# Kernel optimization log

Hardware: AMD Instinct MI355X
Metric: run time of the kernel (lower is better)

Reference implementation:

```python
import jax, jax.numpy as jnp
import numpy as np
import math

M, INPUT_DIM, CLASSES, LATENT = 4096, 64, 10, 2

# ---- Bessel-approximation phi functions (Abramowitz & Stegun polynomial series) ----

def phi_f(s):
    t = s / 7.5
    t2 = t * t
    poly = 1.0 + 3.5156229 * t2 + 3.0899424 * t2**2 + 1.2067492 * t2**3 \
         + 0.2659732 * t2**4 + 0.0360768 * t2**5 + 0.0045813 * t2**6
    return jnp.exp(-s / 2.0) * poly


def phi_g(s):
    t = s / 7.5
    u = 1.0 / t  # s >= 7.5 when called via phi, so t >= 1
    poly = 0.39894228 + 0.01328592 * u + 0.00225319 * u**2 - 0.00157565 * u**3 \
         + 0.0091628 * u**4 - 0.02057706 * u**5 + 0.02635537 * u**6 \
         - 0.01647633 * u**7 + 0.00392377 * u**8
    return jnp.sqrt(2.0 / s) * poly


def phi(x):
    a = jnp.float32(7.5)
    return phi_f(jnp.minimum(x, a)) - phi_f(a) + phi_g(jnp.maximum(x, a))


def phi_d(s, D):
    if D <= 2:
        return phi(s)
    return 1.0 / jnp.sqrt(1.0 + 4.0 * s / (2 * D - 3))


def cramer_wold_distance(X, mu, variance, p, gamma):
    m, K = X.shape
    variance_matrix = variance[None, :] + variance[:, None]          # [C, C]
    # A term: pairwise latent-sample distances [m, m]
    A1 = jnp.sum((X[None, :, :] - X[:, None, :]) ** 2, axis=-1)      # [m, m]
    A = jnp.sum(phi_d(A1 / (4.0 * gamma), K)) / (m * m * math.sqrt(2.0 * math.pi * 2.0 * gamma))
    # B term: sample-to-mean distances [m, C]
    B1 = jnp.sum((mu[None, :, :] - X[:, None, :]) ** 2, axis=-1)     # [m, C]
    B2 = phi_d(B1 / (2.0 * (variance + 2.0 * gamma)), K)
    B = jnp.sum(2.0 * p / (m * jnp.sqrt(2.0 * math.pi * (variance + 2.0 * gamma))) * B2)
    # C term: mean-to-mean distances [C, C]
    C1 = jnp.sum((mu[None, :, :] - mu[:, None, :]) ** 2, axis=-1)
    C2 = phi_d(C1 / (2.0 * variance_matrix + 4.0 * gamma), K)
    C3 = jnp.outer(p, p) / jnp.sqrt(2.0 * math.pi * (variance_matrix + 2.0 * gamma))
    C = jnp.sum(C3 * C2)
    return A - B + C


def setup_inputs() -> dict:
    key = jax.random.key(0)
    ks = jax.random.split(key, 12)
    tau = jax.random.normal(ks[0], (M, INPUT_DIM), dtype=jnp.float32)
    # first half of batch is labeled (one-hot), second half unlabeled (zeros)
    lab_idx = jax.random.randint(ks[1], (M // 2,), 0, CLASSES)
    labels = jnp.concatenate([jax.nn.one_hot(lab_idx, CLASSES, dtype=jnp.float32),
                              jnp.zeros((M - M // 2, CLASSES), jnp.float32)], axis=0)
    batch_data = jnp.concatenate([tau, labels], axis=1)

    def xavier(k, fan_in, fan_out):
        lim = math.sqrt(6.0 / (fan_in + fan_out))
        return jax.random.uniform(k, (fan_in, fan_out), jnp.float32, -lim, lim)

    inp = {
        'batch_data': batch_data,
        'We1': xavier(ks[2], INPUT_DIM, 32), 'be1': jnp.zeros((32,), jnp.float32),
        'We2': xavier(ks[3], 32, 16),        'be2': jnp.zeros((16,), jnp.float32),
        'We3': xavier(ks[4], 16, LATENT),    'be3': jnp.zeros((LATENT,), jnp.float32),
        'Wd1': xavier(ks[5], LATENT, 16),    'bd1': jnp.zeros((16,), jnp.float32),
        'Wd2': xavier(ks[6], 16, 32),        'bd2': jnp.zeros((32,), jnp.float32),
        'Wd3': xavier(ks[7], 32, INPUT_DIM), 'bd3': jnp.zeros((INPUT_DIM,), jnp.float32),
        # GMM: init=2.0, gauss_num <= z_dim branch not taken (10 > 2) -> N(0, init)
        'means': 2.0 * jax.random.normal(ks[8], (CLASSES, LATENT), jnp.float32),
        'variances': jnp.ones((CLASSES,), jnp.float32),
        'probs': jnp.full((CLASSES,), 1.0 / CLASSES, jnp.float32),
    }
    return inp


def segma_forward(batch_data, We1, be1, We2, be2, We3, be3,
                  Wd1, bd1, Wd2, bd2, Wd3, bd3, means, variances, probs):
    tau = batch_data[:, :INPUT_DIM]
    labels = batch_data[:, INPUT_DIM:]
    # encoder
    x = jnp.tanh(tau @ We1 + be1)
    x = jnp.tanh(x @ We2 + be2)
    z = x @ We3 + be3                                               # [m, K]
    # decoder
    h = jnp.tanh(z @ Wd1 + bd1)
    h = jnp.tanh(h @ Wd2 + bd2)
    tau_decoded = h @ Wd3 + bd3
    rec_loss = jnp.mean((tau - tau_decoded) ** 2)
    # labeled mask: rows whose one-hot labels sum to exactly 1
    labeled_mask = (jnp.sum(labels, axis=-1) == 1.0)
    # class logits: Gaussian log-likelihood under each mixture component
    D = means.shape[-1]
    sq = jnp.sum((z[:, None, :] - means[None, :, :]) ** 2, axis=-1)  # [m, C]
    class_logits = jnp.log(probs) - 0.5 * D * jnp.log(2.0 * math.pi * variances) - sq / (2.0 * variances)
    # cross-entropy with (soft/one-hot) float targets, masked to labeled rows
    ce = -jnp.sum(labels * jax.nn.log_softmax(class_logits, axis=-1), axis=-1)
    den = jnp.sum(labels)
    den = jnp.where(den == 0, 1.0, den)
    class_loss = jnp.sum(ce * labeled_mask.astype(jnp.float32)) / den
    # Cramer-Wold cost (train_labeled=True -> use all z)
    m = z.shape[0]
    gamma = jnp.float32((4.0 / (3.0 * m)) ** 0.2)
    cw_cost = cramer_wold_distance(z, means, variances, probs, gamma)
    log_cw_cost = 8.0 + jnp.log(cw_cost)
    total_loss = rec_loss + 1.0 * log_cw_cost + 2.0 * class_loss
    return total_loss


def reference(batch_data, We1, be1, We2, be2, We3, be3,
              Wd1, bd1, Wd2, bd2, Wd3, bd3, means, variances, probs):
    return segma_forward(batch_data, We1, be1, We2, be2, We3, be3,
                         Wd1, bd1, Wd2, bd2, Wd3, bd3, means, variances, probs)
```

## Files before the change

kernel.cpp:

```cpp
#include <hip/hip_runtime.h>
#include <math.h>

#define M_ROWS 4096
#define IN_DIM 64
#define NCLS 10
#define ROW_STRIDE 74
#define TWO_PI_F 6.283185307179586f
#define NTILE 64
#define NPAIR 2080

__device__ __forceinline__ float phi_f_eval(float s) {
    float t = s * (1.0f / 7.5f);
    float t2 = t * t;
    float p = 0.0045813f;
    p = fmaf(p, t2, 0.0360768f);
    p = fmaf(p, t2, 0.2659732f);
    p = fmaf(p, t2, 1.2067492f);
    p = fmaf(p, t2, 3.0899424f);
    p = fmaf(p, t2, 3.5156229f);
    p = fmaf(p, t2, 1.0f);
    return __expf(-0.5f * s) * p;
}

__device__ __forceinline__ float phi_g_eval(float s) {
    float r = __builtin_amdgcn_rcpf(s);
    float u = 7.5f * r;
    float p = 0.00392377f;
    p = fmaf(p, u, -0.01647633f);
    p = fmaf(p, u, 0.02635537f);
    p = fmaf(p, u, -0.02057706f);
    p = fmaf(p, u, 0.0091628f);
    p = fmaf(p, u, -0.00157565f);
    p = fmaf(p, u, 0.00225319f);
    p = fmaf(p, u, 0.01328592f);
    p = fmaf(p, u, 0.39894228f);
    return __builtin_amdgcn_sqrtf(2.0f * r) * p;
}

#define PHI_F_75 0.21445709f

__device__ __forceinline__ float phi_eval(float s) {
    float f = phi_f_eval(fminf(s, 7.5f));
    float g = phi_g_eval(fmaxf(s, 7.5f));
    return f - PHI_F_75 + g;
}

__device__ __forceinline__ float fast_tanh(float x) {
    float e = __expf(2.0f * x);
    float r = __builtin_amdgcn_rcpf(e + 1.0f);
    return fmaf(-2.0f, r, 1.0f);
}

__device__ __forceinline__ float waveReduce(float v) {
    v += __shfl_down(v, 32, 64);
    v += __shfl_down(v, 16, 64);
    v += __shfl_down(v, 8, 64);
    v += __shfl_down(v, 4, 64);
    v += __shfl_down(v, 2, 64);
    v += __shfl_down(v, 1, 64);
    return v;
}

__device__ __forceinline__ double waveReduceD(double v) {
    v += __shfl_down(v, 32, 64);
    v += __shfl_down(v, 16, 64);
    v += __shfl_down(v, 8, 64);
    v += __shfl_down(v, 4, 64);
    v += __shfl_down(v, 2, 64);
    v += __shfl_down(v, 1, 64);
    return v;
}

#define O_W1T   0
#define O_W2T   2048
#define O_WD2T  2560
#define O_WD3T  3072
#define O_W3T   5120
#define O_WD1T  5152
#define O_B1    5184
#define O_B2    5216
#define O_B3    5232
#define O_BD1   5236
#define O_BD2   5252
#define O_BD3   5284
#define O_MU    5348
#define O_VAR   5368
#define O_PRB   5378
#define SM_TOT  5392

__global__ __launch_bounds__(64, 1) void k_mlp(
    const float* __restrict__ batch,
    const float* __restrict__ We1, const float* __restrict__ be1,
    const float* __restrict__ We2, const float* __restrict__ be2,
    const float* __restrict__ We3, const float* __restrict__ be3,
    const float* __restrict__ Wd1, const float* __restrict__ bd1,
    const float* __restrict__ Wd2, const float* __restrict__ bd2,
    const float* __restrict__ Wd3, const float* __restrict__ bd3,
    const float* __restrict__ means, const float* __restrict__ vars,
    const float* __restrict__ probs,
    float2* __restrict__ zbuf,
    float* __restrict__ recp, float* __restrict__ Bp,
    float* __restrict__ clsp, float* __restrict__ labp,
    float gamma)
{
    __shared__ __align__(16) float sm[SM_TOT];
    const int tid = threadIdx.x;

    for (int idx = tid; idx < 2048; idx += 64) { int i = idx >> 5, j = idx & 31; sm[O_W1T + j * 64 + i] = We1[idx]; }
    for (int idx = tid; idx < 512;  idx += 64) { int i = idx >> 4, j = idx & 15; sm[O_W2T + j * 32 + i] = We2[idx]; }
    for (int idx = tid; idx < 512;  idx += 64) { int i = idx >> 5, j = idx & 31; sm[O_WD2T + j * 16 + i] = Wd2[idx]; }
    for (int idx = tid; idx < 2048; idx += 64) { int i = idx >> 6, j = idx & 63; sm[O_WD3T + j * 32 + i] = Wd3[idx]; }
    if (tid < 32) { int i = tid >> 1, j = tid & 1;  sm[O_W3T + j * 16 + i] = We3[tid]; }
    else          { int t2 = tid - 32; int i = t2 >> 4, j = t2 & 15; sm[O_WD1T + j * 2 + i] = Wd1[t2]; }
    if (tid < 32) sm[O_B1 + tid] = be1[tid];
    if (tid < 16) sm[O_B2 + tid] = be2[tid];
    if (tid < 2)  sm[O_B3 + tid] = be3[tid];
    if (tid < 16) sm[O_BD1 + tid] = bd1[tid];
    if (tid < 32) sm[O_BD2 + tid] = bd2[tid];
    sm[O_BD3 + tid] = bd3[tid];
    if (tid < 20) sm[O_MU + tid] = means[tid];
    if (tid < 10) sm[O_VAR + tid] = vars[tid];
    if (tid < 10) sm[O_PRB + tid] = probs[tid];
    __syncthreads();

    const int row = blockIdx.x * 64 + tid;
    const float* rp = batch + (size_t)row * ROW_STRIDE;

    float tau[64];
#pragma unroll
    for (int i = 0; i < 32; i++) {
        float2 v = ((const float2*)rp)[i];
        tau[2 * i] = v.x; tau[2 * i + 1] = v.y;
    }

    float x1[32];
#pragma unroll
    for (int j = 0; j < 32; j++) {
        const float4* w = (const float4*)&sm[O_W1T + j * 64];
        float acc = sm[O_B1 + j];
#pragma unroll
        for (int i = 0; i < 16; i++) {
            float4 wv = w[i];
            acc = fmaf(tau[4 * i],     wv.x, acc);
            acc = fmaf(tau[4 * i + 1], wv.y, acc);
            acc = fmaf(tau[4 * i + 2], wv.z, acc);
            acc = fmaf(tau[4 * i + 3], wv.w, acc);
        }
        x1[j] = fast_tanh(acc);
    }

    float x2[16];
#pragma unroll
    for (int j = 0; j < 16; j++) {
        const float4* w = (const float4*)&sm[O_W2T + j * 32];
        float acc = sm[O_B2 + j];
#pragma unroll
        for (int i = 0; i < 8; i++) {
            float4 wv = w[i];
            acc = fmaf(x1[4 * i],     wv.x, acc);
            acc = fmaf(x1[4 * i + 1], wv.y, acc);
            acc = fmaf(x1[4 * i + 2], wv.z, acc);
            acc = fmaf(x1[4 * i + 3], wv.w, acc);
        }
        x2[j] = fast_tanh(acc);
    }

    float z0 = sm[O_B3 + 0], z1 = sm[O_B3 + 1];
#pragma unroll
    for (int i = 0; i < 16; i++) {
        z0 = fmaf(x2[i], sm[O_W3T + 0 * 16 + i], z0);
        z1 = fmaf(x2[i], sm[O_W3T + 1 * 16 + i], z1);
    }
    zbuf[row] = make_float2(z0, z1);

    float h1[16];
#pragma unroll
    for (int j = 0; j < 16; j++) {
        float acc = sm[O_BD1 + j];
        acc = fmaf(z0, sm[O_WD1T + j * 2 + 0], acc);
        acc = fmaf(z1, sm[O_WD1T + j * 2 + 1], acc);
        h1[j] = fast_tanh(acc);
    }

    float h2[32];
#pragma unroll
    for (int j = 0; j < 32; j++) {
        const float4* w = (const float4*)&sm[O_WD2T + j * 16];
        float acc = sm[O_BD2 + j];
#pragma unroll
        for (int i = 0; i < 4; i++) {
            float4 wv = w[i];
            acc = fmaf(h1[4 * i],     wv.x, acc);
            acc = fmaf(h1[4 * i + 1], wv.y, acc);
            acc = fmaf(h1[4 * i + 2], wv.z, acc);
            acc = fmaf(h1[4 * i + 3], wv.w, acc);
        }
        h2[j] = fast_tanh(acc);
    }

    float rec = 0.0f;
#pragma unroll
    for (int o = 0; o < 64; o++) {
        const float4* w = (const float4*)&sm[O_WD3T + o * 32];
        float acc = sm[O_BD3 + o];
#pragma unroll
        for (int i = 0; i < 8; i++) {
            float4 wv = w[i];
            acc = fmaf(h2[4 * i],     wv.x, acc);
            acc = fmaf(h2[4 * i + 1], wv.y, acc);
            acc = fmaf(h2[4 * i + 2], wv.z, acc);
            acc = fmaf(h2[4 * i + 3], wv.w, acc);
        }
        float e = acc - tau[o];
        rec = fmaf(e, e, rec);
    }

    const float two_g = 2.0f * gamma;
    const float inv_m = 1.0f / (float)M_ROWS;
    float lg[NCLS];
    float mx = -3.0e38f;
    float Bacc = 0.0f;
#pragma unroll
    for (int c = 0; c < NCLS; c++) {
        float d0 = z0 - sm[O_MU + 2 * c];
        float d1 = z1 - sm[O_MU + 2 * c + 1];
        float sqc = fmaf(d0, d0, d1 * d1);
        float vc = sm[O_VAR + c];
        float lgc = __logf(sm[O_PRB + c]) - __logf(TWO_PI_F * vc)
                    - sqc * 0.5f * __builtin_amdgcn_rcpf(vc);
        lg[c] = lgc;
        mx = fmaxf(mx, lgc);

        float den = vc + two_g;
        float sB = sqc * 0.5f * __builtin_amdgcn_rcpf(den);
        float coef = 2.0f * inv_m * sm[O_PRB + c] * __builtin_amdgcn_rsqf(TWO_PI_F * den);
        Bacc = fmaf(coef, phi_eval(sB), Bacc);
    }
    float esum = 0.0f;
#pragma unroll
    for (int c = 0; c < NCLS; c++) esum += __expf(lg[c] - mx);
    float lse = __logf(esum) + mx;

    float suml = 0.0f, ce = 0.0f;
#pragma unroll
    for (int c = 0; c < NCLS; c++) {
        float lb = rp[IN_DIM + c];
        suml += lb;
        ce = fmaf(lb, lse - lg[c], ce);
    }
    float cls = (suml == 1.0f) ? ce : 0.0f;

    float r0 = waveReduce(rec);
    float r1 = waveReduce(Bacc);
    float r2 = waveReduce(cls);
    float r3 = waveReduce(suml);
    if (tid == 0) {
        recp[blockIdx.x] = r0;
        Bp[blockIdx.x]   = r1;
        clsp[blockIdx.x] = r2;
        labp[blockIdx.x] = r3;
    }
}

__global__ __launch_bounds__(64, 4) void k_pair(
    const float2* __restrict__ z, float* __restrict__ Apart, float inv4g)
{
    const int p = blockIdx.x;
    int tj = (int)((__builtin_amdgcn_sqrtf(8.0f * (float)p + 1.0f) - 1.0f) * 0.5f);
    while ((tj + 1) * (tj + 2) / 2 <= p) tj++;
    while (tj * (tj + 1) / 2 > p) tj--;
    const int ti = p - tj * (tj + 1) / 2;

    const int lane = threadIdx.x;
    __shared__ float2 zjs[64];
    float2 zi = z[ti * 64 + lane];
    zjs[lane] = z[tj * 64 + lane];
    __syncthreads();

    float acc0 = 0.0f, acc1 = 0.0f;
#pragma unroll 8
    for (int jj = 0; jj < 64; jj += 2) {
        float2 a = zjs[jj], b = zjs[jj + 1];
        float dx0 = zi.x - a.x, dy0 = zi.y - a.y;
        float dx1 = zi.x - b.x, dy1 = zi.y - b.y;
        acc0 += phi_eval(fmaf(dx0, dx0, dy0 * dy0) * inv4g);
        acc1 += phi_eval(fmaf(dx1, dx1, dy1 * dy1) * inv4g);
    }
    float tot = waveReduce(acc0 + acc1);
    if (lane == 0) Apart[p] = (ti == tj) ? tot : 2.0f * tot;
}

__global__ __launch_bounds__(256) void k_fin(
    const float* __restrict__ means, const float* __restrict__ vars,
    const float* __restrict__ probs,
    const float* __restrict__ Apart,
    const float* __restrict__ recp, const float* __restrict__ Bp,
    const float* __restrict__ clsp, const float* __restrict__ labp,
    float* __restrict__ out, float gamma)
{
    __shared__ double wsum[8];
    const int t = threadIdx.x;
    const int w = t >> 6;

    const double m = (double)M_ROWS;
    const double gam = (double)gamma;
    const double invA = 1.0 / (m * m * sqrt(2.0 * M_PI * 2.0 * gam));

    double av = 0.0;
#pragma unroll
    for (int k = 0; k < 9; k++) {
        int idx = t + 256 * k;
        if (idx < NPAIR) av += (double)Apart[idx];
    }

    double cv = 0.0;
    if (t < 100) {
        int ci = t / 10, cj = t - 10 * (t / 10);
        float vm = vars[ci] + vars[cj];
        float d0 = means[2 * ci] - means[2 * cj];
        float d1 = means[2 * ci + 1] - means[2 * cj + 1];
        float c1 = fmaf(d0, d0, d1 * d1);
        float s = c1 / (2.0f * vm + 4.0f * gamma);
        float c2 = phi_eval(s);
        float c3 = probs[ci] * probs[cj] * __builtin_amdgcn_rsqf(TWO_PI_F * (vm + 2.0f * gamma));
        cv = (double)(c3 * c2);
    }

    double acw = waveReduceD(av * invA + cv);

    const int l = t & 63;
    double pv;
    if (w == 0)      pv = (double)recp[l];
    else if (w == 1) pv = (double)Bp[l];
    else if (w == 2) pv = (double)clsp[l];
    else             pv = (double)labp[l];
    double pw = waveReduceD(pv);

    if (l == 0) { wsum[w] = acw; wsum[4 + w] = pw; }
    __syncthreads();

    if (t == 0) {
        double AC = wsum[0] + wsum[1] + wsum[2] + wsum[3];
        double rec = wsum[4], B = wsum[5], cls = wsum[6], lab = wsum[7];
        double den = (lab == 0.0) ? 1.0 : lab;
        double cw = AC - B;
        double total = rec / (m * 64.0) + 8.0 + log(cw) + 2.0 * (cls / den);
        out[0] = (float)total;
    }
}

extern "C" void kernel_launch(void* const* d_in, const int* in_sizes, int n_in,
                              void* d_out, int out_size, void* d_ws, size_t ws_size,
                              hipStream_t stream) {
    (void)in_sizes; (void)n_in; (void)out_size; (void)ws_size;
    const float* batch = (const float*)d_in[0];
    const float* We1 = (const float*)d_in[1];
    const float* be1 = (const float*)d_in[2];
    const float* We2 = (const float*)d_in[3];
    const float* be2 = (const float*)d_in[4];
    const float* We3 = (const float*)d_in[5];
    const float* be3 = (const float*)d_in[6];
    const float* Wd1 = (const float*)d_in[7];
    const float* bd1 = (const float*)d_in[8];
    const float* Wd2 = (const float*)d_in[9];
    const float* bd2 = (const float*)d_in[10];
    const float* Wd3 = (const float*)d_in[11];
    const float* bd3 = (const float*)d_in[12];
    const float* means = (const float*)d_in[13];
    const float* vars = (const float*)d_in[14];
    const float* probs = (const float*)d_in[15];

    float* ws = (float*)d_ws;
    float2* zbuf = (float2*)ws;
    float* Apart = ws + 8192;
    float* recp  = ws + 12288;
    float* Bp    = ws + 12352;
    float* clsp  = ws + 12416;
    float* labp  = ws + 12480;

    const float gamma = (float)pow(4.0 / (3.0 * (double)M_ROWS), 0.2);
    const float inv4g = 1.0f / (4.0f * gamma);

    k_mlp<<<64, 64, 0, stream>>>(batch, We1, be1, We2, be2, We3, be3,
                                 Wd1, bd1, Wd2, bd2, Wd3, bd3,
                                 means, vars, probs,
                                 zbuf, recp, Bp, clsp, labp, gamma);
    k_pair<<<NPAIR, 64, 0, stream>>>(zbuf, Apart, inv4g);
    k_fin<<<1, 256, 0, stream>>>(means, vars, probs, Apart, recp, Bp, clsp, labp,
                                 (float*)d_out, gamma);
}
```

Measured before the change: 131.4 us.

## Split each MLP row across four lanes with shuffle reductions, use 256 blocks

The encoder/decoder MLP now assigns four lanes per row: each lane handles a quarter of the input features, accumulates partial outputs for all neurons, then combines them with xor shuffles and keeps its own slice of neurons. Weights are stored row-major with padding in shared memory to suit this access pattern. The grid grows from 64 to 256 blocks, so more of the GPU is occupied, and the finisher reads 256 partials per quantity instead of 64. The cost is many extra shuffles per layer, redundant per-row class and B computation across lanes, and more per-lane accumulator registers.

```diff
diff --git a/kernel.cpp b/kernel.cpp
--- a/kernel.cpp
+++ b/kernel.cpp
@@ -8,6 +8,7 @@
 #define TWO_PI_F 6.283185307179586f
 #define NTILE 64
 #define NPAIR 2080
+#define NBLK_MLP 256
 
 __device__ __forceinline__ float phi_f_eval(float s) {
     float t = s * (1.0f / 7.5f);
@@ -71,22 +72,28 @@
     return v;
 }
 
-#define O_W1T   0
-#define O_W2T   2048
-#define O_WD2T  2560
-#define O_WD3T  3072
-#define O_W3T   5120
-#define O_WD1T  5152
-#define O_B1    5184
-#define O_B2    5216
-#define O_B3    5232
-#define O_BD1   5236
-#define O_BD2   5252
-#define O_BD3   5284
-#define O_MU    5348
-#define O_VAR   5368
-#define O_PRB   5378
-#define SM_TOT  5392
+__device__ __forceinline__ float sel4(float v0, float v1, float v2, float v3, int r) {
+    float a = (r & 1) ? v1 : v0;
+    float b = (r & 1) ? v3 : v2;
+    return (r & 2) ? b : a;
+}
+
+#define P_W1   0
+#define P_W2   2304
+#define P_WD2  2944
+#define P_WD3  3520
+#define P_W3   5696
+#define P_WD1  5728
+#define P_B1   5760
+#define P_B2   5792
+#define P_B3   5808
+#define P_BD1  5810
+#define P_BD2  5826
+#define P_BD3  5858
+#define P_MU   5922
+#define P_VAR  5942
+#define P_PRB  5952
+#define SMT    5962
 
 __global__ __launch_bounds__(64, 1) void k_mlp(
     const float* __restrict__ batch,
@@ -103,115 +110,170 @@
     float* __restrict__ clsp, float* __restrict__ labp,
     float gamma)
 {
-    __shared__ __align__(16) float sm[SM_TOT];
+    __shared__ __align__(16) float sm[SMT];
     const int tid = threadIdx.x;
 
-    for (int idx = tid; idx < 2048; idx += 64) { int i = idx >> 5, j = idx & 31; sm[O_W1T + j * 64 + i] = We1[idx]; }
-    for (int idx = tid; idx < 512;  idx += 64) { int i = idx >> 4, j = idx & 15; sm[O_W2T + j * 32 + i] = We2[idx]; }
-    for (int idx = tid; idx < 512;  idx += 64) { int i = idx >> 5, j = idx & 31; sm[O_WD2T + j * 16 + i] = Wd2[idx]; }
-    for (int idx = tid; idx < 2048; idx += 64) { int i = idx >> 6, j = idx & 63; sm[O_WD3T + j * 32 + i] = Wd3[idx]; }
-    if (tid < 32) { int i = tid >> 1, j = tid & 1;  sm[O_W3T + j * 16 + i] = We3[tid]; }
-    else          { int t2 = tid - 32; int i = t2 >> 4, j = t2 & 15; sm[O_WD1T + j * 2 + i] = Wd1[t2]; }
-    if (tid < 32) sm[O_B1 + tid] = be1[tid];
-    if (tid < 16) sm[O_B2 + tid] = be2[tid];
-    if (tid < 2)  sm[O_B3 + tid] = be3[tid];
-    if (tid < 16) sm[O_BD1 + tid] = bd1[tid];
-    if (tid < 32) sm[O_BD2 + tid] = bd2[tid];
-    sm[O_BD3 + tid] = bd3[tid];
-    if (tid < 20) sm[O_MU + tid] = means[tid];
-    if (tid < 10) sm[O_VAR + tid] = vars[tid];
-    if (tid < 10) sm[O_PRB + tid] = probs[tid];
+    for (int idx = tid; idx < 2048; idx += 64) { int i = idx >> 5, j = idx & 31; sm[P_W1  + i * 36 + j] = We1[idx]; }
+    for (int idx = tid; idx < 512;  idx += 64) { int i = idx >> 4, j = idx & 15; sm[P_W2  + i * 20 + j] = We2[idx]; }
+    for (int idx = tid; idx < 512;  idx += 64) { int i = idx >> 5, j = idx & 31; sm[P_WD2 + i * 36 + j] = Wd2[idx]; }
+    for (int idx = tid; idx < 2048; idx += 64) { int i = idx >> 6, j = idx & 63; sm[P_WD3 + i * 68 + j] = Wd3[idx]; }
+    if (tid < 32) sm[P_W3 + tid] = We3[tid];
+    else          sm[P_WD1 + tid - 32] = Wd1[tid - 32];
+    if (tid < 32) sm[P_B1 + tid] = be1[tid];
+    if (tid < 16) sm[P_B2 + tid] = be2[tid];
+    if (tid < 2)  sm[P_B3 + tid] = be3[tid];
+    if (tid < 16) sm[P_BD1 + tid] = bd1[tid];
+    if (tid < 32) sm[P_BD2 + tid] = bd2[tid];
+    sm[P_BD3 + tid] = bd3[tid];
+    if (tid < 20) sm[P_MU + tid] = means[tid];
+    if (tid < 10) sm[P_VAR + tid] = vars[tid];
+    if (tid < 10) sm[P_PRB + tid] = probs[tid];
     __syncthreads();
 
-    const int row = blockIdx.x * 64 + tid;
+    const int rw = tid & 15;
+    const int r  = tid >> 4;
+    const int row = blockIdx.x * 16 + rw;
     const float* rp = batch + (size_t)row * ROW_STRIDE;
 
-    float tau[64];
-#pragma unroll
-    for (int i = 0; i < 32; i++) {
-        float2 v = ((const float2*)rp)[i];
-        tau[2 * i] = v.x; tau[2 * i + 1] = v.y;
-    }
-
-    float x1[32];
+    float taus[16];
+#pragma unroll
+    for (int k = 0; k < 16; k++) taus[k] = rp[r + 4 * k];
+
+    float a1[32];
+#pragma unroll
+    for (int j = 0; j < 32; j++) a1[j] = 0.0f;
+#pragma unroll
+    for (int k = 0; k < 16; k++) {
+        const int i = r + 4 * k;
+        const float4* wr = (const float4*)&sm[P_W1 + i * 36];
+        const float ti = taus[k];
+#pragma unroll
+        for (int jj = 0; jj < 8; jj++) {
+            float4 w = wr[jj];
+            a1[4 * jj + 0] = fmaf(ti, w.x, a1[4 * jj + 0]);
+            a1[4 * jj + 1] = fmaf(ti, w.y, a1[4 * jj + 1]);
+            a1[4 * jj + 2] = fmaf(ti, w.z, a1[4 * jj + 2]);
+            a1[4 * jj + 3] = fmaf(ti, w.w, a1[4 * jj + 3]);
+        }
+    }
 #pragma unroll
     for (int j = 0; j < 32; j++) {
-        const float4* w = (const float4*)&sm[O_W1T + j * 64];
-        float acc = sm[O_B1 + j];
-#pragma unroll
-        for (int i = 0; i < 16; i++) {
-            float4 wv = w[i];
-            acc = fmaf(tau[4 * i],     wv.x, acc);
-            acc = fmaf(tau[4 * i + 1], wv.y, acc);
-            acc = fmaf(tau[4 * i + 2], wv.z, acc);
-            acc = fmaf(tau[4 * i + 3], wv.w, acc);
+        a1[j] += __shfl_xor(a1[j], 16, 64);
+        a1[j] += __shfl_xor(a1[j], 32, 64);
+    }
+    float x1own[8];
+#pragma unroll
+    for (int k = 0; k < 8; k++)
+        x1own[k] = fast_tanh(sel4(a1[4 * k], a1[4 * k + 1], a1[4 * k + 2], a1[4 * k + 3], r)
+                             + sm[P_B1 + r + 4 * k]);
+
+    float a2[16];
+#pragma unroll
+    for (int j = 0; j < 16; j++) a2[j] = 0.0f;
+#pragma unroll
+    for (int k = 0; k < 8; k++) {
+        const int i = r + 4 * k;
+        const float4* wr = (const float4*)&sm[P_W2 + i * 20];
+        const float x = x1own[k];
+#pragma unroll
+        for (int jj = 0; jj < 4; jj++) {
+            float4 w = wr[jj];
+            a2[4 * jj + 0] = fmaf(x, w.x, a2[4 * jj + 0]);
+            a2[4 * jj + 1] = fmaf(x, w.y, a2[4 * jj + 1]);
+            a2[4 * jj + 2] = fmaf(x, w.z, a2[4 * jj + 2]);
+            a2[4 * jj + 3] = fmaf(x, w.w, a2[4 * jj + 3]);
         }
-        x1[j] = fast_tanh(acc);
-    }
-
-    float x2[16];
+    }
 #pragma unroll
     for (int j = 0; j < 16; j++) {
-        const float4* w = (const float4*)&sm[O_W2T + j * 32];
-        float acc = sm[O_B2 + j];
-#pragma unroll
-        for (int i = 0; i < 8; i++) {
-            float4 wv = w[i];
-            acc = fmaf(x1[4 * i],     wv.x, acc);
-            acc = fmaf(x1[4 * i + 1], wv.y, acc);
-            acc = fmaf(x1[4 * i + 2], wv.z, acc);
-            acc = fmaf(x1[4 * i + 3], wv.w, acc);
+        a2[j] += __shfl_xor(a2[j], 16, 64);
+        a2[j] += __shfl_xor(a2[j], 32, 64);
+    }
+    float x2own[4];
+#pragma unroll
+    for (int k = 0; k < 4; k++)
+        x2own[k] = fast_tanh(sel4(a2[4 * k], a2[4 * k + 1], a2[4 * k + 2], a2[4 * k + 3], r)
+                             + sm[P_B2 + r + 4 * k]);
+
+    float z0 = 0.0f, z1 = 0.0f;
+#pragma unroll
+    for (int k = 0; k < 4; k++) {
+        const int i = r + 4 * k;
+        z0 = fmaf(x2own[k], sm[P_W3 + 2 * i], z0);
+        z1 = fmaf(x2own[k], sm[P_W3 + 2 * i + 1], z1);
+    }
+    z0 += __shfl_xor(z0, 16, 64); z0 += __shfl_xor(z0, 32, 64);
+    z1 += __shfl_xor(z1, 16, 64); z1 += __shfl_xor(z1, 32, 64);
+    z0 += sm[P_B3 + 0];
+    z1 += sm[P_B3 + 1];
+    if (r == 0) zbuf[row] = make_float2(z0, z1);
+
+    float h1own[4];
+#pragma unroll
+    for (int k = 0; k < 4; k++) {
+        const int j = r + 4 * k;
+        float acc = sm[P_BD1 + j];
+        acc = fmaf(z0, sm[P_WD1 + j], acc);
+        acc = fmaf(z1, sm[P_WD1 + 16 + j], acc);
+        h1own[k] = fast_tanh(acc);
+    }
+
+    float a3[32];
+#pragma unroll
+    for (int j = 0; j < 32; j++) a3[j] = 0.0f;
+#pragma unroll
+    for (int k = 0; k < 4; k++) {
+        const int i = r + 4 * k;
+        const float4* wr = (const float4*)&sm[P_WD2 + i * 36];
+        const float x = h1own[k];
+#pragma unroll
+        for (int jj = 0; jj < 8; jj++) {
+            float4 w = wr[jj];
+            a3[4 * jj + 0] = fmaf(x, w.x, a3[4 * jj + 0]);
+            a3[4 * jj + 1] = fmaf(x, w.y, a3[4 * jj + 1]);
+            a3[4 * jj + 2] = fmaf(x, w.z, a3[4 * jj + 2]);
+            a3[4 * jj + 3] = fmaf(x, w.w, a3[4 * jj + 3]);
         }
-        x2[j] = fast_tanh(acc);
-    }
-
-    float z0 = sm[O_B3 + 0], z1 = sm[O_B3 + 1];
-#pragma unroll
-    for (int i = 0; i < 16; i++) {
-        z0 = fmaf(x2[i], sm[O_W3T + 0 * 16 + i], z0);
-        z1 = fmaf(x2[i], sm[O_W3T + 1 * 16 + i], z1);
-    }
-    zbuf[row] = make_float2(z0, z1);
-
-    float h1[16];
-#pragma unroll
-    for (int j = 0; j < 16; j++) {
-        float acc = sm[O_BD1 + j];
-        acc = fmaf(z0, sm[O_WD1T + j * 2 + 0], acc);
-        acc = fmaf(z1, sm[O_WD1T + j * 2 + 1], acc);
-        h1[j] = fast_tanh(acc);
-    }
-
-    float h2[32];
+    }
 #pragma unroll
     for (int j = 0; j < 32; j++) {
-        const float4* w = (const float4*)&sm[O_WD2T + j * 16];
-        float acc = sm[O_BD2 + j];
-#pragma unroll
-        for (int i = 0; i < 4; i++) {
-            float4 wv = w[i];
-            acc = fmaf(h1[4 * i],     wv.x, acc);
-            acc = fmaf(h1[4 * i + 1], wv.y, acc);
-            acc = fmaf(h1[4 * i + 2], wv.z, acc);
-            acc = fmaf(h1[4 * i + 3], wv.w, acc);
+        a3[j] += __shfl_xor(a3[j], 16, 64);
+        a3[j] += __shfl_xor(a3[j], 32, 64);
+    }
+    float h2own[8];
+#pragma unroll
+    for (int k = 0; k < 8; k++)
+        h2own[k] = fast_tanh(sel4(a3[4 * k], a3[4 * k + 1], a3[4 * k + 2], a3[4 * k + 3], r)
+                             + sm[P_BD2 + r + 4 * k]);
+
+    float a4[64];
+#pragma unroll
+    for (int j = 0; j < 64; j++) a4[j] = 0.0f;
+#pragma unroll
+    for (int k = 0; k < 8; k++) {
+        const int i = r + 4 * k;
+        const float4* wr = (const float4*)&sm[P_WD3 + i * 68];
+        const float x = h2own[k];
+#pragma unroll
+        for (int jj = 0; jj < 16; jj++) {
+            float4 w = wr[jj];
+            a4[4 * jj + 0] = fmaf(x, w.x, a4[4 * jj + 0]);
+            a4[4 * jj + 1] = fmaf(x, w.y, a4[4 * jj + 1]);
+            a4[4 * jj + 2] = fmaf(x, w.z, a4[4 * jj + 2]);
+            a4[4 * jj + 3] = fmaf(x, w.w, a4[4 * jj + 3]);
         }
-        h2[j] = fast_tanh(acc);
-    }
-
+    }
+#pragma unroll
+    for (int j = 0; j < 64; j++) {
+        a4[j] += __shfl_xor(a4[j], 16, 64);
+        a4[j] += __shfl_xor(a4[j], 32, 64);
+    }
     float rec = 0.0f;
 #pragma unroll
-    for (int o = 0; o < 64; o++) {
-        const float4* w = (const float4*)&sm[O_WD3T + o * 32];
-        float acc = sm[O_BD3 + o];
-#pragma unroll
-        for (int i = 0; i < 8; i++) {
-            float4 wv = w[i];
-            acc = fmaf(h2[4 * i],     wv.x, acc);
-            acc = fmaf(h2[4 * i + 1], wv.y, acc);
-            acc = fmaf(h2[4 * i + 2], wv.z, acc);
-            acc = fmaf(h2[4 * i + 3], wv.w, acc);
-        }
-        float e = acc - tau[o];
+    for (int k = 0; k < 16; k++) {
+        float dec = sel4(a4[4 * k], a4[4 * k + 1], a4[4 * k + 2], a4[4 * k + 3], r)
+                    + sm[P_BD3 + r + 4 * k];
+        float e = dec - taus[k];
         rec = fmaf(e, e, rec);
     }
 
@@ -222,18 +284,18 @@
     float Bacc = 0.0f;
 #pragma unroll
     for (int c = 0; c < NCLS; c++) {
-        float d0 = z0 - sm[O_MU + 2 * c];
-        float d1 = z1 - sm[O_MU + 2 * c + 1];
+        float d0 = z0 - sm[P_MU + 2 * c];
+        float d1 = z1 - sm[P_MU + 2 * c + 1];
         float sqc = fmaf(d0, d0, d1 * d1);
-        float vc = sm[O_VAR + c];
-        float lgc = __logf(sm[O_PRB + c]) - __logf(TWO_PI_F * vc)
+        float vc = sm[P_VAR + c];
+        float lgc = __logf(sm[P_PRB + c]) - __logf(TWO_PI_F * vc)
                     - sqc * 0.5f * __builtin_amdgcn_rcpf(vc);
         lg[c] = lgc;
         mx = fmaxf(mx, lgc);
 
         float den = vc + two_g;
         float sB = sqc * 0.5f * __builtin_amdgcn_rcpf(den);
-        float coef = 2.0f * inv_m * sm[O_PRB + c] * __builtin_amdgcn_rsqf(TWO_PI_F * den);
+        float coef = 2.0f * inv_m * sm[P_PRB + c] * __builtin_amdgcn_rsqf(TWO_PI_F * den);
         Bacc = fmaf(coef, phi_eval(sB), Bacc);
     }
     float esum = 0.0f;
@@ -249,6 +311,7 @@
         ce = fmaf(lb, lse - lg[c], ce);
     }
     float cls = (suml == 1.0f) ? ce : 0.0f;
+    if (r != 0) { Bacc = 0.0f; cls = 0.0f; suml = 0.0f; }
 
     float r0 = waveReduce(rec);
     float r1 = waveReduce(Bacc);
@@ -301,6 +364,7 @@
     __shared__ double wsum[8];
     const int t = threadIdx.x;
     const int w = t >> 6;
+    const int l = t & 63;
 
     const double m = (double)M_ROWS;
     const double gam = (double)gamma;
@@ -328,12 +392,10 @@
 
     double acw = waveReduceD(av * invA + cv);
 
-    const int l = t & 63;
-    double pv;
-    if (w == 0)      pv = (double)recp[l];
-    else if (w == 1) pv = (double)Bp[l];
-    else if (w == 2) pv = (double)clsp[l];
-    else             pv = (double)labp[l];
+    const float* arr = (w == 0) ? recp : (w == 1) ? Bp : (w == 2) ? clsp : labp;
+    double pv = 0.0;
+#pragma unroll
+    for (int k = 0; k < 4; k++) pv += (double)arr[l + 64 * k];
     double pw = waveReduceD(pv);
 
     if (l == 0) { wsum[w] = acw; wsum[4 + w] = pw; }
@@ -374,17 +436,17 @@
     float2* zbuf = (float2*)ws;
     float* Apart = ws + 8192;
     float* recp  = ws + 12288;
-    float* Bp    = ws + 12352;
-    float* clsp  = ws + 12416;
-    float* labp  = ws + 12480;
+    float* Bp    = ws + 12544;
+    float* clsp  = ws + 12800;
+    float* labp  = ws + 13056;
 
     const float gamma = (float)pow(4.0 / (3.0 * (double)M_ROWS), 0.2);
     const float inv4g = 1.0f / (4.0f * gamma);
 
-    k_mlp<<<64, 64, 0, stream>>>(batch, We1, be1, We2, be2, We3, be3,
-                                 Wd1, bd1, Wd2, bd2, Wd3, bd3,
-                                 means, vars, probs,
-                                 zbuf, recp, Bp, clsp, labp, gamma);
+    k_mlp<<<NBLK_MLP, 64, 0, stream>>>(batch, We1, be1, We2, be2, We3, be3,
+                                       Wd1, bd1, Wd2, bd2, Wd3, bd3,
+                                       means, vars, probs,
+                                       zbuf, recp, Bp, clsp, labp, gamma);
     k_pair<<<NPAIR, 64, 0, stream>>>(zbuf, Apart, inv4g);
     k_fin<<<1, 256, 0, stream>>>(means, vars, probs, Apart, recp, Bp, clsp, labp,
                                  (float*)d_out, gamma);
```

New measurement: 116.9 us. 1.12x faster.
